# Kernel optimization log

Hardware: AMD Instinct MI355X
Metric: run time of the kernel (lower is better)

The kernel has to match this reference:

```python
import jax, jax.numpy as jnp
import numpy as np

INTERVAL = 0.5  # voxel_size_ratio
N_RAYS = 131072
M_SAMPLES = 8388608  # ~64 samples per ray on average
ALPHA_INIT = 0.01


def setup_inputs() -> dict:
    key = jax.random.key(0)
    k1, k2, k3 = jax.random.split(key, 3)
    density = jax.random.normal(k1, (M_SAMPLES,), jnp.float32)
    rgb_feat = jax.random.normal(k2, (M_SAMPLES, 3), jnp.float32)  # raw k0 colors
    # act_shift buffer: log(1/(1-alpha_init) - 1)
    shift = jnp.array([np.log(1.0 / (1.0 - ALPHA_INIT) - 1.0)], jnp.float32)
    # sorted ray ids (samples along each ray are contiguous, near->far)
    ray_id = jnp.sort(jax.random.randint(k3, (M_SAMPLES,), 0, N_RAYS)).astype(jnp.int32)
    return {"density": density, "rgb_feat": rgb_feat, "shift": shift,
            "ray_id": ray_id, "N": N_RAYS}


def reference(density, rgb_feat, shift, ray_id, N):
    # Raw2Alpha: alpha = 1 - (1 + exp(density + shift))^(-interval)
    #          = 1 - exp(-softplus(density + shift) * interval)
    sp = jax.nn.softplus(density + shift[0])
    log1ma = -sp * INTERVAL            # log(1 - alpha), exact
    alpha = 1.0 - jnp.exp(log1ma)

    # Alphas2Weights: per-ray exclusive cumulative product of (1 - alpha)
    # done in log space with a segmented exclusive cumsum.
    seg_tot = jax.ops.segment_sum(log1ma, ray_id, num_segments=N)   # [N] log prod per ray
    seg_excl = jnp.cumsum(seg_tot) - seg_tot                        # log prod of previous rays
    within_excl = jnp.cumsum(log1ma) - log1ma - seg_excl[ray_id]    # exclusive within segment
    T = jnp.exp(within_excl)          # transmittance before each sample
    weights = alpha * T               # [M]
    alphainv_last = jnp.exp(seg_tot)  # [N] leftover transmittance per ray

    # composite colors per ray + white-ish background via alphainv_last
    rgb = jax.nn.sigmoid(rgb_feat)
    rgb_marched = jax.ops.segment_sum(weights[:, None] * rgb, ray_id, num_segments=N)
    out = rgb_marched + alphainv_last[:, None]   # [N, 3]
    return weights, alphainv_last, out
```

## Files before the change

kernel.cpp:

```cpp
#include <hip/hip_runtime.h>


__device__ __forceinline__ float fast_sigmoid(float x) {
    return __builtin_amdgcn_rcpf(1.0f + __expf(-x));
}

#define DPP_ADD(x, ctrl, rmask)                                               \
    do {                                                                      \
        int _s = __builtin_amdgcn_update_dpp(0, __float_as_int(x), (ctrl),    \
                                             (rmask), 0xf, true);             \
        (x) += __int_as_float(_s);                                            \
    } while (0)

#define DPP_MUL(x, ctrl, rmask)                                               \
    do {                                                                      \
        int _s = __builtin_amdgcn_update_dpp(0x3f800000, __float_as_int(x),   \
                                             (ctrl), (rmask), 0xf, false);    \
        (x) *= __int_as_float(_s);                                            \
    } while (0)

__device__ __forceinline__ float wave_scan_add(float x) {
    DPP_ADD(x, 0x111, 0xf);
    DPP_ADD(x, 0x112, 0xf);
    DPP_ADD(x, 0x114, 0xf);
    DPP_ADD(x, 0x118, 0xf);
    DPP_ADD(x, 0x142, 0xa);
    DPP_ADD(x, 0x143, 0xc);
    return x;
}

__device__ __forceinline__ float wave_scan_mul(float x) {
    DPP_MUL(x, 0x111, 0xf);
    DPP_MUL(x, 0x112, 0xf);
    DPP_MUL(x, 0x114, 0xf);
    DPP_MUL(x, 0x118, 0xf);
    DPP_MUL(x, 0x142, 0xa);
    DPP_MUL(x, 0x143, 0xc);
    return x;
}

__device__ __forceinline__ float bcast_lane63(float x) {
    return __int_as_float(__builtin_amdgcn_readlane(__float_as_int(x), 63));
}

__global__ __launch_bounds__(256) void seg_starts4_kernel(
    const int4* __restrict__ ray4, int M4, int M, int N,
    const int* __restrict__ ray_id, int* __restrict__ starts)
{
    const int i = blockIdx.x * blockDim.x + threadIdx.x;
    if (i >= M4) return;
    const int4 v = ray4[i];
    const int prev = (i == 0) ? -1 : ray_id[4 * i - 1];
    const int base = 4 * i;
    for (int r = prev + 1; r <= v.x; ++r) starts[r] = base;
    for (int r = v.x + 1;  r <= v.y; ++r) starts[r] = base + 1;
    for (int r = v.y + 1;  r <= v.z; ++r) starts[r] = base + 2;
    for (int r = v.z + 1;  r <= v.w; ++r) starts[r] = base + 3;
    if (i == M4 - 1) {
        int last = v.w;
        for (int j = 4 * M4; j < M; ++j) {
            const int cur = ray_id[j];
            for (int r = last + 1; r <= cur; ++r) starts[r] = j;
            last = cur;
        }
        for (int r = last + 1; r <= N; ++r) starts[r] = M;
    }
}

__global__ __launch_bounds__(256) void favor_render_kernel(
    const float* __restrict__ density,
    const float* __restrict__ rgb_feat,
    const float* __restrict__ shift,
    const int*   __restrict__ starts,
    int M, int N,
    float* __restrict__ weights,
    float* __restrict__ alphainv_last,
    float* __restrict__ out3)
{
    const int wave = (blockIdx.x * blockDim.x + threadIdx.x) >> 6;
    const int t    = threadIdx.x & 63;
    if (wave >= N) return;
    const int ray = wave;

    const int start = starts[ray];
    const int end   = starts[ray + 1];

    const float sh = shift[0];

    float carryT = 1.0f;
    float acc0 = 0.0f, acc1 = 0.0f, acc2 = 0.0f;

    for (int base = start; base < end; base += 128) {
        const int i0 = base + t;
        const int i1 = i0 + 64;
        const bool v0 = (i0 < end);
        const bool v1 = (i1 < end);
        const bool any1 = (base + 64) < end;

        const int c0 = min(i0, end - 1);
        const float d0 = density[c0];
        const float r0 = rgb_feat[3 * c0 + 0];
        const float g0 = rgb_feat[3 * c0 + 1];
        const float b0 = rgb_feat[3 * c0 + 2];
        float d1 = 0.0f, r1 = 0.0f, g1 = 0.0f, b1 = 0.0f;
        if (any1) {
            const int c1 = min(i1, end - 1);
            d1 = density[c1];
            r1 = rgb_feat[3 * c1 + 0];
            g1 = rgb_feat[3 * c1 + 1];
            b1 = rgb_feat[3 * c1 + 2];
        }

        const float u0 = 1.0f + __expf(d0 + sh);
        const float a0 = __builtin_amdgcn_rsqf(u0);
        const float m0 = v0 ? a0 : 1.0f;
        const float s0 = wave_scan_mul(m0);
        const float tot0 = bcast_lane63(s0);
        const float Ti0  = carryT * s0;
        const float w0   = Ti0 * (u0 * a0 - 1.0f);
        if (v0) {
            weights[i0] = w0;
            acc0 += w0 * fast_sigmoid(r0);
            acc1 += w0 * fast_sigmoid(g0);
            acc2 += w0 * fast_sigmoid(b0);
        }

        if (any1) {
            const float u1 = 1.0f + __expf(d1 + sh);
            const float a1 = __builtin_amdgcn_rsqf(u1);
            const float m1 = v1 ? a1 : 1.0f;
            const float s1 = wave_scan_mul(m1);
            const float tot1 = bcast_lane63(s1);
            const float Ti1  = carryT * tot0 * s1;
            const float w1   = Ti1 * (u1 * a1 - 1.0f);
            if (v1) {
                weights[i1] = w1;
                acc0 += w1 * fast_sigmoid(r1);
                acc1 += w1 * fast_sigmoid(g1);
                acc2 += w1 * fast_sigmoid(b1);
            }
            carryT *= tot0 * tot1;
        } else {
            carryT *= tot0;
        }
    }

    const float s_acc0 = bcast_lane63(wave_scan_add(acc0));
    const float s_acc1 = bcast_lane63(wave_scan_add(acc1));
    const float s_acc2 = bcast_lane63(wave_scan_add(acc2));

    if (t == 0) {
        const float ainv = carryT;
        alphainv_last[ray] = ainv;
        out3[3 * ray + 0] = s_acc0 + ainv;
        out3[3 * ray + 1] = s_acc1 + ainv;
        out3[3 * ray + 2] = s_acc2 + ainv;
    }
}

extern "C" void kernel_launch(void* const* d_in, const int* in_sizes, int n_in,
                              void* d_out, int out_size, void* d_ws, size_t ws_size,
                              hipStream_t stream) {
    const float* density  = (const float*)d_in[0];
    const float* rgb_feat = (const float*)d_in[1];
    const float* shift    = (const float*)d_in[2];
    const int*   ray_id   = (const int*)d_in[3];

    const int M = in_sizes[0];
    const int N = (out_size - M) / 4;

    float* weights       = (float*)d_out;
    float* alphainv_last = weights + M;
    float* out3          = alphainv_last + N;

    const int block = 256;
    int* starts = (int*)d_ws;

    const int M4 = M >> 2;
    const int grid_starts = (M4 + block - 1) / block;
    seg_starts4_kernel<<<grid_starts, block, 0, stream>>>(
        (const int4*)ray_id, M4, M, N, ray_id, starts);

    const int grid_render = (N * 64 + block - 1) / block;
    favor_render_kernel<<<grid_render, block, 0, stream>>>(
        density, rgb_feat, shift, starts, M, N,
        weights, alphainv_last, out3);
}
```

Baseline: 220.8 us.

## Process four rays per wave with prefetched first-chunk loads

Each wave now handles four consecutive rays instead of one. It reads all five segment boundaries with a single load plus readlane, and issues the first 64-sample chunk loads for all four rays up front so their memory latency overlaps. Later chunks of each ray are processed 64 at a time instead of the previous 128-wide unrolled step. This cuts the wave count and per-ray setup overhead in exchange for less parallelism across waves and serialised ray processing within a wave. Rays longer than 64 samples (the average is 64) fall into a slower dependent loop.

Measured after the change: 214.1 us. 1.03x faster.

```diff
diff --git a/kernel.cpp b/kernel.cpp
--- a/kernel.cpp
+++ b/kernel.cpp
@@ -67,6 +67,8 @@
     }
 }
 
+#define RPW 4
+
 __global__ __launch_bounds__(256) void favor_render_kernel(
     const float* __restrict__ density,
     const float* __restrict__ rgb_feat,
@@ -79,82 +81,85 @@
 {
     const int wave = (blockIdx.x * blockDim.x + threadIdx.x) >> 6;
     const int t    = threadIdx.x & 63;
-    if (wave >= N) return;
-    const int ray = wave;
+    const int r0   = wave * RPW;
+    if (r0 >= N) return;
 
-    const int start = starts[ray];
-    const int end   = starts[ray + 1];
+    const int bv = starts[min(r0 + t, N)];
+    int s[RPW + 1];
+    #pragma unroll
+    for (int k = 0; k <= RPW; ++k)
+        s[k] = __builtin_amdgcn_readlane(bv, k);
 
     const float sh = shift[0];
 
-    float carryT = 1.0f;
-    float acc0 = 0.0f, acc1 = 0.0f, acc2 = 0.0f;
+    float pd[RPW], pr[RPW], pg[RPW], pb[RPW];
+    #pragma unroll
+    for (int j = 0; j < RPW; ++j) {
+        const int c = max(min(s[j] + t, s[j + 1] - 1), 0);
+        pd[j] = density[c];
+        pr[j] = rgb_feat[3 * c + 0];
+        pg[j] = rgb_feat[3 * c + 1];
+        pb[j] = rgb_feat[3 * c + 2];
+    }
 
-    for (int base = start; base < end; base += 128) {
-        const int i0 = base + t;
-        const int i1 = i0 + 64;
-        const bool v0 = (i0 < end);
-        const bool v1 = (i1 < end);
-        const bool any1 = (base + 64) < end;
+    #pragma unroll
+    for (int j = 0; j < RPW; ++j) {
+        const int ray = r0 + j;
+        if (ray >= N) continue;
+        const int st = s[j], en = s[j + 1];
 
-        const int c0 = min(i0, end - 1);
-        const float d0 = density[c0];
-        const float r0 = rgb_feat[3 * c0 + 0];
-        const float g0 = rgb_feat[3 * c0 + 1];
-        const float b0 = rgb_feat[3 * c0 + 2];
-        float d1 = 0.0f, r1 = 0.0f, g1 = 0.0f, b1 = 0.0f;
-        if (any1) {
-            const int c1 = min(i1, end - 1);
-            d1 = density[c1];
-            r1 = rgb_feat[3 * c1 + 0];
-            g1 = rgb_feat[3 * c1 + 1];
-            b1 = rgb_feat[3 * c1 + 2];
+        float carryT = 1.0f;
+        float a0 = 0.0f, a1 = 0.0f, a2 = 0.0f;
+
+        {
+            const bool valid = (st + t) < en;
+            const float u = 1.0f + __expf(pd[j] + sh);
+            const float a = __builtin_amdgcn_rsqf(u);
+            const float m = valid ? a : 1.0f;
+            const float S = wave_scan_mul(m);
+            const float tot = bcast_lane63(S);
+            const float w = S * (u * a - 1.0f);
+            if (valid) {
+                weights[st + t] = w;
+                a0 = w * fast_sigmoid(pr[j]);
+                a1 = w * fast_sigmoid(pg[j]);
+                a2 = w * fast_sigmoid(pb[j]);
+            }
+            carryT = tot;
         }
 
-        const float u0 = 1.0f + __expf(d0 + sh);
-        const float a0 = __builtin_amdgcn_rsqf(u0);
-        const float m0 = v0 ? a0 : 1.0f;
-        const float s0 = wave_scan_mul(m0);
-        const float tot0 = bcast_lane63(s0);
-        const float Ti0  = carryT * s0;
-        const float w0   = Ti0 * (u0 * a0 - 1.0f);
-        if (v0) {
-            weights[i0] = w0;
-            acc0 += w0 * fast_sigmoid(r0);
-            acc1 += w0 * fast_sigmoid(g0);
-            acc2 += w0 * fast_sigmoid(b0);
+        for (int base = st + 64; base < en; base += 64) {
+            const int i = base + t;
+            const bool valid = i < en;
+            const int c = min(i, en - 1);
+            const float d = density[c];
+            const float r = rgb_feat[3 * c + 0];
+            const float g = rgb_feat[3 * c + 1];
+            const float b = rgb_feat[3 * c + 2];
+            const float u = 1.0f + __expf(d + sh);
+            const float a = __builtin_amdgcn_rsqf(u);
+            const float m = valid ? a : 1.0f;
+            const float S = wave_scan_mul(m);
+            const float tot = bcast_lane63(S);
+            const float w = carryT * S * (u * a - 1.0f);
+            if (valid) {
+                weights[i] = w;
+                a0 += w * fast_sigmoid(r);
+                a1 += w * fast_sigmoid(g);
+                a2 += w * fast_sigmoid(b);
+            }
+            carryT *= tot;
         }
 
-        if (any1) {
-            const float u1 = 1.0f + __expf(d1 + sh);
-            const float a1 = __builtin_amdgcn_rsqf(u1);
-            const float m1 = v1 ? a1 : 1.0f;
-            const float s1 = wave_scan_mul(m1);
-            const float tot1 = bcast_lane63(s1);
-            const float Ti1  = carryT * tot0 * s1;
-            const float w1   = Ti1 * (u1 * a1 - 1.0f);
-            if (v1) {
-                weights[i1] = w1;
-                acc0 += w1 * fast_sigmoid(r1);
-                acc1 += w1 * fast_sigmoid(g1);
-                acc2 += w1 * fast_sigmoid(b1);
-            }
-            carryT *= tot0 * tot1;
-        } else {
-            carryT *= tot0;
+        const float t0 = bcast_lane63(wave_scan_add(a0));
+        const float t1 = bcast_lane63(wave_scan_add(a1));
+        const float t2 = bcast_lane63(wave_scan_add(a2));
+        if (t == 0) {
+            alphainv_last[ray] = carryT;
+            out3[3 * ray + 0] = t0 + carryT;
+            out3[3 * ray + 1] = t1 + carryT;
+            out3[3 * ray + 2] = t2 + carryT;
         }
-    }
-
-    const float s_acc0 = bcast_lane63(wave_scan_add(acc0));
-    const float s_acc1 = bcast_lane63(wave_scan_add(acc1));
-    const float s_acc2 = bcast_lane63(wave_scan_add(acc2));
-
-    if (t == 0) {
-        const float ainv = carryT;
-        alphainv_last[ray] = ainv;
-        out3[3 * ray + 0] = s_acc0 + ainv;
-        out3[3 * ray + 1] = s_acc1 + ainv;
-        out3[3 * ray + 2] = s_acc2 + ainv;
     }
 }
 
@@ -181,7 +186,8 @@
     seg_starts4_kernel<<<grid_starts, block, 0, stream>>>(
         (const int4*)ray_id, M4, M, N, ray_id, starts);
 
-    const int grid_render = (N * 64 + block - 1) / block;
+    const int n_waves = (N + RPW - 1) / RPW;
+    const int grid_render = (n_waves * 64 + block - 1) / block;
     favor_render_kernel<<<grid_render, block, 0, stream>>>(
         density, rgb_feat, shift, starts, M, N,
         weights, alphainv_last, out3);
```
